# Kernel optimization log

Measured on AMD Instinct MI355X. Metric: run time of the kernel, lower is better.

## Reference

```python
import jax, jax.numpy as jnp
import numpy as np

E, G, NL, NC, NLP, NPTS = 256, 8, 4, 6, 6, 13
GD = E // G
FIX_SCALE = jnp.array([[0,0,0],[0.45,0,0],[-0.45,0,0],[0,0.45,0],[0,-0.45,0],[0,0,0.45],[0,0,-0.45]], dtype=jnp.float32)
FM_SHAPES = [(64,176),(32,88),(16,44),(8,22)]

def linear(x, w, b):
    return x @ w + b

def layernorm(x, g, b):
    m = x.mean(-1, keepdims=True)
    v = ((x - m) ** 2).mean(-1, keepdims=True)
    return (x - m) * jax.lax.rsqrt(v + 1e-5) * g + b

def grid_sample_bilinear(fm, grid):
    # fm: [B,C,H,W], grid: [B,Hg,Wg,2] in [-1,1]; align_corners=False, zero padding
    B, C, H, W = fm.shape
    gx = (grid[..., 0] + 1.0) * (W * 0.5) - 0.5
    gy = (grid[..., 1] + 1.0) * (H * 0.5) - 0.5
    x0f = jnp.floor(gx); y0f = jnp.floor(gy)
    wx1 = gx - x0f; wy1 = gy - y0f
    x0 = x0f.astype(jnp.int32); y0 = y0f.astype(jnp.int32)
    def samp(fmb, x, y):
        valid = ((x >= 0) & (x < W) & (y >= 0) & (y < H)).astype(fmb.dtype)
        xc = jnp.clip(x, 0, W - 1); yc = jnp.clip(y, 0, H - 1)
        return fmb[:, yc, xc] * valid[None]
    def per_batch(fmb, x0b, y0b, wx1b, wy1b):
        wx0 = 1.0 - wx1b; wy0 = 1.0 - wy1b
        v00 = samp(fmb, x0b, y0b)
        v01 = samp(fmb, x0b + 1, y0b)
        v10 = samp(fmb, x0b, y0b + 1)
        v11 = samp(fmb, x0b + 1, y0b + 1)
        return (v00 * (wx0 * wy0)[None] + v01 * (wx1b * wy0)[None]
                + v10 * (wx0 * wy1b)[None] + v11 * (wx1b * wy1b)[None])
    return jax.vmap(per_batch)(fm, x0, y0, wx1, wy1)

def setup_inputs() -> dict:
    key = jax.random.key(0)
    ks = jax.random.split(key, 32)
    bs, na = 2, 900
    inp = {
        'instance_feature': jax.random.normal(ks[0], (bs, na, E), jnp.float32),
        'anchor': jax.random.normal(ks[1], (bs, na, 11), jnp.float32),
        'anchor_embed': jax.random.normal(ks[2], (bs, na, E), jnp.float32),
        'projection_mat': jax.random.normal(ks[3], (bs, NC, 4, 4), jnp.float32),
        'image_wh': jnp.ones((bs, NC, 2), jnp.float32) * jnp.array([704.0, 256.0]),
    }
    for i, (h, w) in enumerate(FM_SHAPES):
        inp[f'fm{i}'] = jax.random.normal(ks[4 + i], (bs, NC, E, h, w), jnp.float32)
    s = 0.02
    inp['lfc_w'] = s * jax.random.normal(ks[10], (E, NLP * 3), jnp.float32)
    inp['lfc_b'] = jnp.zeros((NLP * 3,), jnp.float32)
    inp['ce1_w'] = s * jax.random.normal(ks[11], (12, E), jnp.float32)
    inp['ce1_b'] = jnp.zeros((E,), jnp.float32)
    inp['ln1_g'] = jnp.ones((E,), jnp.float32)
    inp['ln1_b'] = jnp.zeros((E,), jnp.float32)
    inp['ce2_w'] = s * jax.random.normal(ks[12], (E, E), jnp.float32)
    inp['ce2_b'] = jnp.zeros((E,), jnp.float32)
    inp['ln2_g'] = jnp.ones((E,), jnp.float32)
    inp['ln2_b'] = jnp.zeros((E,), jnp.float32)
    inp['wfc_w'] = s * jax.random.normal(ks[13], (E, G * NL * NPTS), jnp.float32)
    inp['wfc_b'] = jnp.zeros((G * NL * NPTS,), jnp.float32)
    inp['op_w'] = s * jax.random.normal(ks[14], (E, E), jnp.float32)
    inp['op_b'] = jnp.zeros((E,), jnp.float32)
    return inp

def reference(instance_feature, anchor, anchor_embed, fm0, fm1, fm2, fm3,
              projection_mat, image_wh,
              lfc_w, lfc_b, ce1_w, ce1_b, ln1_g, ln1_b, ce2_w, ce2_b,
              ln2_g, ln2_b, wfc_w, wfc_b, op_w, op_b):
    bs, na = instance_feature.shape[:2]
    # ---- keypoint generator ----
    size = jnp.exp(anchor[..., None, 3:6])                      # [bs,na,1,3] (W,L,H)
    kp = FIX_SCALE * size                                       # [bs,na,7,3]
    ls = jax.nn.sigmoid(linear(instance_feature, lfc_w, lfc_b)).reshape(bs, na, NLP, 3) - 0.5
    kp = jnp.concatenate([kp, ls * size], axis=-2)              # [bs,na,13,3]
    sy, cy = anchor[..., 6], anchor[..., 7]
    zero, one = jnp.zeros_like(cy), jnp.ones_like(cy)
    rot = jnp.stack([jnp.stack([cy, -sy, zero], -1),
                     jnp.stack([sy, cy, zero], -1),
                     jnp.stack([zero, zero, one], -1)], axis=-2)  # [bs,na,3,3]
    key_points = jnp.einsum('bnij,bnpj->bnpi', rot, kp) + anchor[..., None, 0:3]
    # ---- weights ----
    feat = instance_feature + anchor_embed
    cam_in = projection_mat[:, :, :3].reshape(bs, NC, 12)
    ce = layernorm(jax.nn.relu(linear(cam_in, ce1_w, ce1_b)), ln1_g, ln1_b)
    ce = layernorm(jax.nn.relu(linear(ce, ce2_w, ce2_b)), ln2_g, ln2_b)   # [bs,nc,E]
    fcam = feat[:, :, None] + ce[:, None]                        # [bs,na,nc,E]
    w = linear(fcam, wfc_w, wfc_b).reshape(bs, na, NC * NL * NPTS, G)
    w = jax.nn.softmax(w, axis=-2).reshape(bs, na, NC, NL, NPTS, G)
    # ---- projection + sampling ----
    pts = jnp.concatenate([key_points, jnp.ones_like(key_points[..., :1])], -1)  # [bs,na,np,4]
    pts2d = jnp.einsum('bcij,bnpj->bcnpi', projection_mat, pts)  # [bs,nc,na,np,4]
    z = jnp.maximum(pts2d[..., 2:3], 1e-5)
    uv = pts2d[..., :2] / z
    uv = uv / image_wh[:, :, None, None]
    grid = (uv * 2.0 - 1.0).reshape(bs * NC, na, NPTS, 2)
    feats = []
    for fm in (fm0, fm1, fm2, fm3):
        h, ww = fm.shape[-2:]
        feats.append(grid_sample_bilinear(fm.reshape(bs * NC, E, h, ww), grid))  # [bs*nc,E,na,np]
    feats = jnp.stack(feats, axis=1).reshape(bs, NC, NL, E, na, NPTS)
    feats = feats.transpose(0, 4, 1, 2, 5, 3)                    # [bs,na,nc,nl,np,E]
    # ---- fusion (sum over cams, levels, pts) ----
    featg = feats.reshape(bs, na, NC, NL, NPTS, G, GD)
    fused = jnp.einsum('bnclpg,bnclpgd->bngd', w, featg).reshape(bs, na, E)
    out = linear(fused, op_w, op_b)
    return jnp.concatenate([out, instance_feature], axis=-1)
```

## Files before the change

kernel.cpp:

```cpp
#include <hip/hip_runtime.h>
#include <hip/hip_bf16.h>

typedef __hip_bfloat16 bf16;
typedef unsigned short ushort_t;
typedef unsigned int uint_t;

#define E    256
#define Gn   8
#define NLv  4
#define NCam 6
#define NP   13
#define BSz  2
#define NA   900
#define NW   416
#define NQ   312
#define NCW  2496

#define NT_BLK   2808
#define PREP_BLK 1800
#define CE_BLK   12

__device__ __forceinline__ float cvt(float v) { return v; }
__device__ __forceinline__ float cvt(bf16 v)  { return __bfloat162float(v); }
__device__ __forceinline__ ushort_t f2us(float v) {
  bf16 h = __float2bfloat16(v);
  return *(ushort_t*)&h;
}
__device__ __forceinline__ float blo(uint_t d) { return __uint_as_float(d << 16); }
__device__ __forceinline__ float bhi(uint_t d) { return __uint_as_float(d & 0xffff0000u); }
__device__ __forceinline__ bool is_f32(const void* wh) {
  return *(const uint_t*)wh == 0x44300000u;
}

constexpr float FIXS[7][3] = {
    {0.f,0.f,0.f},{0.45f,0.f,0.f},{-0.45f,0.f,0.f},
    {0.f,0.45f,0.f},{0.f,-0.45f,0.f},{0.f,0.f,0.45f},{0.f,0.f,-0.45f}};
__constant__ int LH_c[4]  = {64,32,16,8};
__constant__ int LW_c[4]  = {176,88,44,22};
__constant__ int LHW_c[4] = {11264,2816,704,176};
__constant__ int PXB_c[4] = {0,135168,168960,177408};
__constant__ size_t TB_c[4]  = {0ull, 34603008ull, 43253760ull, 45416448ull};

struct CEShared {
  float cin[12];
  float xs[E];
  float red[E];
};

template<typename T>
__device__ void camembed_bce_body(CEShared* sm, int bc,
    const T* __restrict__ pm,
    const T* __restrict__ ce1_w, const T* __restrict__ ce1_b,
    const T* __restrict__ ln1_g, const T* __restrict__ ln1_b,
    const T* __restrict__ ce2_w, const T* __restrict__ ce2_b,
    const T* __restrict__ ln2_g, const T* __restrict__ ln2_b,
    const T* __restrict__ wfc_w, float* __restrict__ bce) {
  const int t  = threadIdx.x;
  float* cin = sm->cin; float* xs = sm->xs; float* red = sm->red;
  if (t < 12) cin[t] = cvt(pm[bc*16 + t]);
  __syncthreads();
  float h = cvt(ce1_b[t]);
#pragma unroll
  for (int k = 0; k < 12; ++k) h = fmaf(cin[k], cvt(ce1_w[k*E + t]), h);
  h = fmaxf(h, 0.f);
  red[t] = h; __syncthreads();
  for (int off = 128; off > 0; off >>= 1) { if (t < off) red[t] += red[t+off]; __syncthreads(); }
  float m = red[0] * (1.f/E); __syncthreads();
  float d = h - m;
  red[t] = d*d; __syncthreads();
  for (int off = 128; off > 0; off >>= 1) { if (t < off) red[t] += red[t+off]; __syncthreads(); }
  float v = red[0] * (1.f/E); __syncthreads();
  xs[t] = d * rsqrtf(v + 1e-5f) * cvt(ln1_g[t]) + cvt(ln1_b[t]);
  __syncthreads();
  float h2 = cvt(ce2_b[t]);
  for (int k = 0; k < E; ++k) h2 = fmaf(xs[k], cvt(ce2_w[k*E + t]), h2);
  h2 = fmaxf(h2, 0.f);
  red[t] = h2; __syncthreads();
  for (int off = 128; off > 0; off >>= 1) { if (t < off) red[t] += red[t+off]; __syncthreads(); }
  float m2 = red[0] * (1.f/E); __syncthreads();
  float d2 = h2 - m2;
  red[t] = d2*d2; __syncthreads();
  for (int off = 128; off > 0; off >>= 1) { if (t < off) red[t] += red[t+off]; __syncthreads(); }
  float v2 = red[0] * (1.f/E);
  __syncthreads();
  xs[t] = d2 * rsqrtf(v2 + 1e-5f) * cvt(ln2_g[t]) + cvt(ln2_b[t]);
  __syncthreads();
  for (int j = t; j < NW; j += E) {
    float s = 0.f;
    for (int k = 0; k < E; ++k) s = fmaf(xs[k], cvt(wfc_w[(size_t)k*NW + j]), s);
    bce[bc*NW + j] = s;
  }
}

struct alignas(16) PWShared2 {
  float rec[NQ*8];
  float instL[E];
  float feat[E];
  float P[96];
  float whs[12];
  float anc[11];
  float ls[18];
};

template<typename T>
__device__ void prep_body(PWShared2* sm, int bn,
    const T* __restrict__ inst, const T* __restrict__ anchor,
    const T* __restrict__ aemb, const T* __restrict__ pm, const T* __restrict__ wh,
    const T* __restrict__ lfc_w, const T* __restrict__ lfc_b,
    const T* __restrict__ wfc_w, const T* __restrict__ wfc_b,
    float* __restrict__ recs_g, float* __restrict__ A_g) {
  const int b = bn / NA;
  const int t = threadIdx.x;
  float* instL = sm->instL; float* feat = sm->feat;
  float* rec = sm->rec; float* P = sm->P; float* whs = sm->whs;
  float* anc = sm->anc; float* ls = sm->ls;

  const float iv = cvt(inst[(size_t)bn*E + t]);
  instL[t] = iv;
  feat[t]  = iv + cvt(aemb[(size_t)bn*E + t]);
  if (t < 96)        P[t]       = cvt(pm[(size_t)b*96 + t]);
  else if (t < 108)  whs[t-96]  = cvt(wh[(size_t)b*12 + (t-96)]);
  else if (t < 119)  anc[t-108] = cvt(anchor[(size_t)bn*11 + (t-108)]);
  __syncthreads();

  {
    float a00=0.f, a01=0.f, a02=0.f, a03=0.f;
    float a10=0.f, a11=0.f, a12=0.f, a13=0.f;
    const bool two = (t < NW - E);
    for (int k = 0; k < E; k += 4) {
      const float f0 = feat[k], f1 = feat[k+1], f2 = feat[k+2], f3 = feat[k+3];
      a00 = fmaf(f0, cvt(wfc_w[(size_t)(k+0)*NW + t]), a00);
      a01 = fmaf(f1, cvt(wfc_w[(size_t)(k+1)*NW + t]), a01);
      a02 = fmaf(f2, cvt(wfc_w[(size_t)(k+2)*NW + t]), a02);
      a03 = fmaf(f3, cvt(wfc_w[(size_t)(k+3)*NW + t]), a03);
      if (two) {
        a10 = fmaf(f0, cvt(wfc_w[(size_t)(k+0)*NW + E + t]), a10);
        a11 = fmaf(f1, cvt(wfc_w[(size_t)(k+1)*NW + E + t]), a11);
        a12 = fmaf(f2, cvt(wfc_w[(size_t)(k+2)*NW + E + t]), a12);
        a13 = fmaf(f3, cvt(wfc_w[(size_t)(k+3)*NW + E + t]), a13);
      }
    }
    A_g[(size_t)bn*NW + t] = (a00+a01) + (a02+a03) + cvt(wfc_b[t]);
    if (two) A_g[(size_t)bn*NW + E + t] = (a10+a11) + (a12+a13) + cvt(wfc_b[E + t]);
  }
  if (t < 18) {
    float s = cvt(lfc_b[t]);
#pragma unroll 8
    for (int k = 0; k < E; ++k) s = fmaf(instL[k], cvt(lfc_w[(size_t)k*18 + t]), s);
    ls[t] = 1.f/(1.f + expf(-s)) - 0.5f;
  }
  __syncthreads();

  if (t < NP) {
    const float s0 = expf(anc[3]), s1 = expf(anc[4]), s2 = expf(anc[5]);
    float kx, ky, kz;
    if (t < 7) { kx = FIXS[t][0]*s0; ky = FIXS[t][1]*s1; kz = FIXS[t][2]*s2; }
    else { const int q = (t-7)*3; kx = ls[q]*s0; ky = ls[q+1]*s1; kz = ls[q+2]*s2; }
    const float sy = anc[6], cy = anc[7];
    const float wx = cy*kx - sy*ky + anc[0];
    const float wy = sy*kx + cy*ky + anc[1];
    const float wz = kz + anc[2];
    for (int c = 0; c < NCam; ++c) {
      const float* Pc = &P[c*16];
      const float px = Pc[0]*wx + Pc[1]*wy + Pc[2]*wz  + Pc[3];
      const float py = Pc[4]*wx + Pc[5]*wy + Pc[6]*wz  + Pc[7];
      const float pz = Pc[8]*wx + Pc[9]*wy + Pc[10]*wz + Pc[11];
      const float z  = fmaxf(pz, 1e-5f);
      const float u  = px / z / whs[c*2+0];
      const float v  = py / z / whs[c*2+1];
#pragma unroll
      for (int l = 0; l < NLv; ++l) {
        const int Wl_ = LW_c[l], Hl = LH_c[l];
        const float fx = u * (float)Wl_ - 0.5f;
        const float fy = v * (float)Hl  - 0.5f;
        const float x0f = floorf(fx), y0f = floorf(fy);
        const int x0 = (int)x0f, y0 = (int)y0f;
        const float wx1 = fx - x0f, wy1 = fy - y0f;
        const float wx0 = 1.f - wx1, wy0 = 1.f - wy1;
        const bool vx0 = (x0 >= 0) && (x0 < Wl_);
        const bool vx1 = (x0+1 >= 0) && (x0+1 < Wl_);
        const bool vy0 = (y0 >= 0) && (y0 < Hl);
        const bool vy1 = (y0+1 >= 0) && (y0+1 < Hl);
        const int x0c = min(max(x0,0),Wl_-1), x1c = min(max(x0+1,0),Wl_-1);
        const int y0c = min(max(y0,0),Hl-1),  y1c = min(max(y0+1,0),Hl-1);
        const int bpx = PXB_c[l] + (b*NCam + c)*LHW_c[l];
        float* r = &rec[((c*NLv + l)*NP + t)*8];
        ((int*)r)[0] = bpx + y0c*Wl_ + x0c;
        ((int*)r)[1] = bpx + y0c*Wl_ + x1c;
        ((int*)r)[2] = bpx + y1c*Wl_ + x0c;
        ((int*)r)[3] = bpx + y1c*Wl_ + x1c;
        r[4] = (vx0 && vy0) ? wx0*wy0 : 0.f;
        r[5] = (vx1 && vy0) ? wx1*wy0 : 0.f;
        r[6] = (vx0 && vy1) ? wx0*wy1 : 0.f;
        r[7] = (vx1 && vy1) ? wx1*wy1 : 0.f;
      }
    }
  }
  __syncthreads();

  float* ro = recs_g + (size_t)bn * (NQ*8);
  for (int i = t; i < NQ*2; i += 256)
    ((float4*)ro)[i] = ((const float4*)rec)[i];
}

struct TRShared { ushort_t tile[64][64]; };

template<typename T>
__device__ void transpose_tile(TRShared* sm, const T* __restrict__ fm,
                               bf16* __restrict__ tfm, int HW, int bc, int p0) {
  const int t = threadIdx.x;
  ushort_t (*tile)[64] = sm->tile;
  ushort_t* tfmu = (ushort_t*)tfm;
  const int sub = t & 15;
  const int grp = t >> 4;
  const int pq  = p0 + sub*4;
  const bool pv = (pq < HW);
#pragma unroll
  for (int cb = 0; cb < 4; ++cb) {
#pragma unroll
    for (int j = 0; j < 4; ++j) {
      const int chl = grp + j*16;
      const int ch  = cb*64 + chl;
      ushort4 v;
      if (pv) {
        const size_t base = (size_t)(bc*E + ch)*HW + pq;
        if constexpr (sizeof(T) == 2) {
          v = *(const ushort4*)((const ushort_t*)fm + base);
        } else {
          const float4 vf = *(const float4*)((const float*)fm + base);
          v.x = f2us(vf.x); v.y = f2us(vf.y); v.z = f2us(vf.z); v.w = f2us(vf.w);
        }
      } else {
        v.x = 0; v.y = 0; v.z = 0; v.w = 0;
      }
      const int qw = sub ^ ((chl >> 2) & 7);
      *(ushort4*)&tile[chl][qw << 2] = v;
    }
    __syncthreads();
    const int ch4 = sub << 2;
    const int swz = sub & 7;
#pragma unroll
    for (int j = 0; j < 4; ++j) {
      const int pxl = grp + j*16;
      const int p = p0 + pxl;
      if (p < HW) {
        const int col = (((pxl >> 2) ^ swz) << 2) + (pxl & 3);
        ushort4 o;
        o.x = tile[ch4+0][col];
        o.y = tile[ch4+1][col];
        o.z = tile[ch4+2][col];
        o.w = tile[ch4+3][col];
        *(ushort4*)(tfmu + ((size_t)bc*HW + p)*E + cb*64 + ch4) = o;
      }
    }
    __syncthreads();
  }
}

__device__ __forceinline__ void tr_decode(int g, int& lvl, int& bc, int& tile) {
  if (g < 2112)      { lvl = 0; bc = g / 176; tile = g - bc*176; }
  else if (g < 2640) { g -= 2112; lvl = 1; bc = g / 44; tile = g - bc*44; }
  else if (g < 2772) { g -= 2640; lvl = 2; bc = g / 11; tile = g - bc*11; }
  else               { g -= 2772; lvl = 3; bc = g / 3;  tile = g - bc*3; }
}

struct alignas(16) FusedSM {
  union { TRShared tr; PWShared2 pw; CEShared ce; } u;
};

__global__ __launch_bounds__(256) void k_stage_all(
    const void* inst, const void* anchor, const void* aemb, const void* pm, const void* wh,
    const void* fm0, const void* fm1, const void* fm2, const void* fm3,
    const void* lfc_w, const void* lfc_b,
    const void* ce1_w, const void* ce1_b, const void* ln1_g, const void* ln1_b,
    const void* ce2_w, const void* ce2_b, const void* ln2_g, const void* ln2_b,
    const void* wfc_w, const void* wfc_b,
    bf16* tfm, float* recs_g, float* A_g, float* bce) {
  __shared__ FusedSM sm;
  const bool f32 = is_f32(wh);
  const int g = blockIdx.x;
  if (g < CE_BLK) {
    if (f32)
      camembed_bce_body<float>(&sm.u.ce, g, (const float*)pm, (const float*)ce1_w,
        (const float*)ce1_b, (const float*)ln1_g, (const float*)ln1_b,
        (const float*)ce2_w, (const float*)ce2_b, (const float*)ln2_g,
        (const float*)ln2_b, (const float*)wfc_w, bce);
    else
      camembed_bce_body<bf16>(&sm.u.ce, g, (const bf16*)pm, (const bf16*)ce1_w,
        (const bf16*)ce1_b, (const bf16*)ln1_g, (const bf16*)ln1_b,
        (const bf16*)ce2_w, (const bf16*)ce2_b, (const bf16*)ln2_g,
        (const bf16*)ln2_b, (const bf16*)wfc_w, bce);
    return;
  }
  const int gi = g - CE_BLK;
  bool isT; int idx;
  if (gi < 4500) {
    const int grp = gi / 5, r = gi - grp*5;
    if (r < 3) { isT = true;  idx = grp*3 + r; }
    else       { isT = false; idx = grp*2 + (r - 3); }
  } else {
    isT = true; idx = 2700 + (gi - 4500);
  }
  if (isT) {
    int lvl, bc, tile;
    tr_decode(idx, lvl, bc, tile);
    const void* fms[4] = {fm0, fm1, fm2, fm3};
    const void* fm = fms[lvl];
    const int HW = LHW_c[lvl];
    bf16* out = tfm + TB_c[lvl];
    if (f32) transpose_tile<float>(&sm.u.tr, (const float*)fm, out, HW, bc, tile*64);
    else     transpose_tile<bf16>(&sm.u.tr, (const bf16*)fm, out, HW, bc, tile*64);
  } else {
    if (f32)
      prep_body<float>(&sm.u.pw, idx, (const float*)inst, (const float*)anchor,
        (const float*)aemb, (const float*)pm, (const float*)wh,
        (const float*)lfc_w, (const float*)lfc_b,
        (const float*)wfc_w, (const float*)wfc_b, recs_g, A_g);
    else
      prep_body<bf16>(&sm.u.pw, idx, (const bf16*)inst, (const bf16*)anchor,
        (const bf16*)aemb, (const bf16*)pm, (const bf16*)wh,
        (const bf16*)lfc_w, (const bf16*)lfc_b,
        (const bf16*)wfc_w, (const bf16*)wfc_b, recs_g, A_g);
  }
}

struct alignas(16) GOShared2 {
  float rec[NQ*8];
  float Wl[NCW];
  float red4f[8*E];
  float red[512];
  float inv8[8];
};

template<typename T>
__device__ void gather_body2(GOShared2* sm,
    const float* __restrict__ recs, const float* __restrict__ A_g,
    const float* __restrict__ bce, const bf16* __restrict__ tfm,
    const T* __restrict__ inst, const T* __restrict__ op_w, const T* __restrict__ op_b,
    T* __restrict__ outp) {
  const int bn = blockIdx.x; const int b = bn / NA;
  const int t = threadIdx.x; const int lane = t & 63; const int wv = t >> 6;
  const int g8 = lane >> 3; const int gg = t & 7;
  float* rec = sm->rec; float* Wl = sm->Wl;
  float* red4f = sm->red4f; float* red = sm->red; float* inv8 = sm->inv8;

  {
    const float* rsrc = recs + (size_t)bn * (NQ*8);
    for (int i = t; i < NQ*2; i += 512) ((float4*)rec)[i] = ((const float4*)rsrc)[i];
    const float* Ab = A_g + (size_t)bn * NW;
    const float* bb = bce + (size_t)(b*NCam) * NW;
    for (int f = t; f < NCW; f += 512) {
      const int c = f / NW, j = f - c*NW;
      Wl[f] = Ab[j] + bb[c*NW + j];
    }
  }
  __syncthreads();

  float mx = -1e30f;
  for (int f = t; f < NCW; f += 512) mx = fmaxf(mx, Wl[f]);
  red[t] = mx; __syncthreads();
  for (int off = 256; off >= 8; off >>= 1) { if (t < off) red[t] = fmaxf(red[t], red[t+off]); __syncthreads(); }
  const float mg = red[gg]; __syncthreads();
  float sum = 0.f;
  for (int f = t; f < NCW; f += 512) { const float e = expf(Wl[f] - mg); Wl[f] = e; sum += e; }
  red[t] = sum; __syncthreads();
  for (int off = 256; off >= 8; off >>= 1) { if (t < off) red[t] += red[t+off]; __syncthreads(); }
  if (t < 8) inv8[t] = 1.f / red[t];
  __syncthreads();

  const ushort_t* tf = (const ushort_t*)tfm;
  const uint_t chg = (uint_t)(lane * 4);
  const float invg = inv8[g8];
  float a0 = 0.f, a1 = 0.f, a2 = 0.f, a3 = 0.f;
  int qi = wv;
  int4   off = *(const int4*)(&rec[qi*8]);
  float4 cw  = *(const float4*)(&rec[qi*8 + 4]);
  float  eq  = Wl[qi*8 + g8];
#pragma unroll 2
  for (int i = 0; i < 39; ++i) {
    const uint2 s00 = *(const uint2*)(tf + ((uint_t)off.x*256u + chg));
    const uint2 s01 = *(const uint2*)(tf + ((uint_t)off.y*256u + chg));
    const uint2 s10 = *(const uint2*)(tf + ((uint_t)off.z*256u + chg));
    const uint2 s11 = *(const uint2*)(tf + ((uint_t)off.w*256u + chg));
    const float c0 = cw.x*eq, c1 = cw.y*eq, c2 = cw.z*eq, c3 = cw.w*eq;
    if (i + 1 < 39) {
      const int qn = qi + 8;
      off = *(const int4*)(&rec[qn*8]);
      cw  = *(const float4*)(&rec[qn*8 + 4]);
      eq  = Wl[qn*8 + g8];
      qi = qn;
    }
    a0 = fmaf(c0, blo(s00.x), a0); a0 = fmaf(c1, blo(s01.x), a0);
    a0 = fmaf(c2, blo(s10.x), a0); a0 = fmaf(c3, blo(s11.x), a0);
    a1 = fmaf(c0, bhi(s00.x), a1); a1 = fmaf(c1, bhi(s01.x), a1);
    a1 = fmaf(c2, bhi(s10.x), a1); a1 = fmaf(c3, bhi(s11.x), a1);
    a2 = fmaf(c0, blo(s00.y), a2); a2 = fmaf(c1, blo(s01.y), a2);
    a2 = fmaf(c2, blo(s10.y), a2); a2 = fmaf(c3, blo(s11.y), a2);
    a3 = fmaf(c0, bhi(s00.y), a3); a3 = fmaf(c1, bhi(s01.y), a3);
    a3 = fmaf(c2, bhi(s10.y), a3); a3 = fmaf(c3, bhi(s11.y), a3);
  }
  a0 *= invg; a1 *= invg; a2 *= invg; a3 *= invg;
  *(float4*)&red4f[(wv << 8) + (lane << 2)] = make_float4(a0, a1, a2, a3);
  __syncthreads();

  if (t < E) {
    float fl = red4f[t];
#pragma unroll
    for (int k = 1; k < 8; ++k) fl += red4f[k*E + t];
    red[t] = fl;
  }
  __syncthreads();
  if (t < E) {
    float o0=0.f, o1=0.f, o2=0.f, o3=0.f;
    for (int k = 0; k < E; k += 4) {
      o0 = fmaf(red[k+0], cvt(op_w[(size_t)(k+0)*E + t]), o0);
      o1 = fmaf(red[k+1], cvt(op_w[(size_t)(k+1)*E + t]), o1);
      o2 = fmaf(red[k+2], cvt(op_w[(size_t)(k+2)*E + t]), o2);
      o3 = fmaf(red[k+3], cvt(op_w[(size_t)(k+3)*E + t]), o3);
    }
    const float o = (o0+o1) + (o2+o3) + cvt(op_b[t]);
    outp[(size_t)bn*512 + t] = (T)o;
  } else {
    const int tt = t - E;
    outp[(size_t)bn*512 + E + tt] = inst[(size_t)bn*E + tt];
  }
}

__global__ __launch_bounds__(512, 6) void k_gather_out2(
    const float* recs, const float* A_g, const float* bce, const bf16* tfm,
    const void* inst, const void* op_w, const void* op_b, const void* wh,
    void* outp) {
  __shared__ GOShared2 sm;
  if (is_f32(wh))
    gather_body2<float>(&sm, recs, A_g, bce, tfm, (const float*)inst,
                        (const float*)op_w, (const float*)op_b, (float*)outp);
  else
    gather_body2<bf16>(&sm, recs, A_g, bce, tfm, (const bf16*)inst,
                       (const bf16*)op_w, (const bf16*)op_b, (bf16*)outp);
}

__global__ __launch_bounds__(256) void k_camembed_bce(
    const void* pm, const void* ce1_w, const void* ce1_b,
    const void* ln1_g, const void* ln1_b, const void* ce2_w, const void* ce2_b,
    const void* ln2_g, const void* ln2_b, const void* wfc_w,
    const void* wh, float* bce) {
  __shared__ CEShared sm;
  if (is_f32(wh))
    camembed_bce_body<float>(&sm, blockIdx.x, (const float*)pm,(const float*)ce1_w,(const float*)ce1_b,
      (const float*)ln1_g,(const float*)ln1_b,(const float*)ce2_w,(const float*)ce2_b,
      (const float*)ln2_g,(const float*)ln2_b,(const float*)wfc_w, bce);
  else
    camembed_bce_body<bf16>(&sm, blockIdx.x, (const bf16*)pm,(const bf16*)ce1_w,(const bf16*)ce1_b,
      (const bf16*)ln1_g,(const bf16*)ln1_b,(const bf16*)ce2_w,(const bf16*)ce2_b,
      (const bf16*)ln2_g,(const bf16*)ln2_b,(const bf16*)wfc_w, bce);
}

__global__ __launch_bounds__(256) void k_transpose_all(
    const void* fm0, const void* fm1, const void* fm2, const void* fm3,
    bf16* tfm, const void* wh) {
  __shared__ TRShared sm;
  int lvl, bc, tile;
  tr_decode(blockIdx.x, lvl, bc, tile);
  const void* fms[4] = {fm0, fm1, fm2, fm3};
  const void* fm = fms[lvl];
  const int HW = LHW_c[lvl];
  bf16* out = tfm + TB_c[lvl];
  if (is_f32(wh)) transpose_tile<float>(&sm, (const float*)fm, out, HW, bc, tile*64);
  else            transpose_tile<bf16>(&sm, (const bf16*)fm, out, HW, bc, tile*64);
}

struct alignas(16) MFShared {
  float rec[NQ*8];
  float Wl[NCW];
  float WT[NCW];
  float feat[E];
  float A[NW];
  float red[E];
  float fusedl[E];
  float P[96];
  float whs[12];
  float anc[11];
  float ls[18];
};

__device__ __forceinline__ float gatherT_f(
    const float* __restrict__ rec, const float* __restrict__ wrowbase,
    const bf16* __restrict__ tfm, int b, int t) {
  float acc = 0.f;
  for (int c = 0; c < NCam; ++c) {
#pragma unroll
    for (int l = 0; l < NLv; ++l) {
      const float* wrow = wrowbase + (c*NLv + l)*NP;
      const float* rb   = rec + (c*NLv + l)*NP*8;
      const int HWl = LHW_c[l];
      const bf16* base = tfm + TB_c[l] + ((size_t)(b*NCam + c) * HWl) * E + t;
#pragma unroll
      for (int p = 0; p < NP; ++p) {
        const int4   off = *(const int4*)(rb + p*8);
        const float4 cw  = *(const float4*)(rb + p*8 + 4);
        const float v = cw.x*cvt(base[(size_t)off.x*E]) + cw.y*cvt(base[(size_t)off.y*E])
                      + cw.z*cvt(base[(size_t)off.z*E]) + cw.w*cvt(base[(size_t)off.w*E]);
        acc = fmaf(wrow[p], v, acc);
      }
    }
  }
  return acc;
}

template<typename T>
__device__ __forceinline__ float gatherD_f(
    const float* __restrict__ rec, const float* __restrict__ wrowbase,
    const T* __restrict__ f0, const T* __restrict__ f1,
    const T* __restrict__ f2, const T* __restrict__ f3, int b, int t) {
  const T* fms[4] = {f0, f1, f2, f3};
  float acc = 0.f;
  for (int c = 0; c < NCam; ++c) {
#pragma unroll
    for (int l = 0; l < NLv; ++l) {
      const float* wrow = wrowbase + (c*NLv + l)*NP;
      const float* rb   = rec + (c*NLv + l)*NP*8;
      const int HWl = LHW_c[l];
      const T* base = fms[l] + ((size_t)(b*NCam + c)*E + t) * HWl;
#pragma unroll
      for (int p = 0; p < NP; ++p) {
        const int4   off = *(const int4*)(rb + p*8);
        const float4 cw  = *(const float4*)(rb + p*8 + 4);
        const float v = cw.x*cvt(base[off.x]) + cw.y*cvt(base[off.y])
                      + cw.z*cvt(base[off.z]) + cw.w*cvt(base[off.w]);
        acc = fmaf(wrow[p], v, acc);
      }
    }
  }
  return acc;
}

template<typename T, bool TRANS>
__device__ void main_body(MFShared* sm,
    const T* __restrict__ inst, const T* __restrict__ anchor,
    const T* __restrict__ aemb, const T* __restrict__ pm, const T* __restrict__ wh,
    const T* __restrict__ fm0, const T* __restrict__ fm1,
    const T* __restrict__ fm2, const T* __restrict__ fm3,
    const T* __restrict__ lfc_w, const T* __restrict__ lfc_b,
    const T* __restrict__ wfc_w, const T* __restrict__ wfc_b,
    const T* __restrict__ op_w, const T* __restrict__ op_b,
    const float* __restrict__ bce, const bf16* __restrict__ tfm,
    T* __restrict__ outp) {
  const int bn = blockIdx.x, b = bn / NA, t = threadIdx.x;
  float* anc = sm->anc; float* P = sm->P; float* whs = sm->whs; float* ls = sm->ls;
  float* rec = sm->rec; float* feat = sm->feat; float* A = sm->A;
  float* Wl = sm->Wl; float* WT = sm->WT; float* red = sm->red; float* fusedl = sm->fusedl;

  feat[t] = cvt(inst[(size_t)bn*E + t]) + cvt(aemb[(size_t)bn*E + t]);
  if (t < 96)               P[t]       = cvt(pm[(size_t)b*96 + t]);
  else if (t < 108)         whs[t-96]  = cvt(wh[(size_t)b*12 + (t-96)]);
  else if (t < 119)         anc[t-108] = cvt(anchor[(size_t)bn*11 + (t-108)]);
  if (t >= 128 && t < 146) {
    const int j = t - 128;
    float s = cvt(lfc_b[j]);
    for (int k = 0; k < E; ++k)
      s = fmaf(cvt(inst[(size_t)bn*E + k]), cvt(lfc_w[(size_t)k*18 + j]), s);
    ls[j] = 1.f/(1.f + expf(-s)) - 0.5f;
  }
  __syncthreads();
  {
    float a0 = cvt(wfc_b[t]);
    for (int k = 0; k < E; ++k) a0 = fmaf(feat[k], cvt(wfc_w[(size_t)k*NW + t]), a0);
    A[t] = a0;
    if (t < NW - E) {
      float a1 = cvt(wfc_b[E + t]);
      for (int k = 0; k < E; ++k) a1 = fmaf(feat[k], cvt(wfc_w[(size_t)k*NW + E + t]), a1);
      A[E + t] = a1;
    }
  }
  if (t < NP) {
    const float s0 = expf(anc[3]), s1 = expf(anc[4]), s2 = expf(anc[5]);
    float kx, ky, kz;
    if (t < 7) { kx = FIXS[t][0]*s0; ky = FIXS[t][1]*s1; kz = FIXS[t][2]*s2; }
    else { const int q = (t-7)*3; kx = ls[q]*s0; ky = ls[q+1]*s1; kz = ls[q+2]*s2; }
    const float sy = anc[6], cy = anc[7];
    const float wx = cy*kx - sy*ky + anc[0];
    const float wy = sy*kx + cy*ky + anc[1];
    const float wz = kz + anc[2];
    for (int c = 0; c < NCam; ++c) {
      const float* Pc = &P[c*16];
      const float px = Pc[0]*wx + Pc[1]*wy + Pc[2]*wz  + Pc[3];
      const float py = Pc[4]*wx + Pc[5]*wy + Pc[6]*wz  + Pc[7];
      const float pz = Pc[8]*wx + Pc[9]*wy + Pc[10]*wz + Pc[11];
      const float z  = fmaxf(pz, 1e-5f);
      const float u  = px / z / whs[c*2+0];
      const float v  = py / z / whs[c*2+1];
#pragma unroll
      for (int l = 0; l < NLv; ++l) {
        const int Wl_ = LW_c[l], Hl = LH_c[l];
        const float fx = u * (float)Wl_ - 0.5f;
        const float fy = v * (float)Hl  - 0.5f;
        const float x0f = floorf(fx), y0f = floorf(fy);
        const int x0 = (int)x0f, y0 = (int)y0f;
        const float wx1 = fx - x0f, wy1 = fy - y0f;
        const float wx0 = 1.f - wx1, wy0 = 1.f - wy1;
        const bool vx0 = (x0 >= 0) && (x0 < Wl_);
        const bool vx1 = (x0+1 >= 0) && (x0+1 < Wl_);
        const bool vy0 = (y0 >= 0) && (y0 < Hl);
        const bool vy1 = (y0+1 >= 0) && (y0+1 < Hl);
        const int x0c = min(max(x0,0),Wl_-1), x1c = min(max(x0+1,0),Wl_-1);
        const int y0c = min(max(y0,0),Hl-1),  y1c = min(max(y0+1,0),Hl-1);
        float* r = &rec[((c*NLv + l)*NP + t)*8];
        ((int*)r)[0] = y0c*Wl_ + x0c;
        ((int*)r)[1] = y0c*Wl_ + x1c;
        ((int*)r)[2] = y1c*Wl_ + x0c;
        ((int*)r)[3] = y1c*Wl_ + x1c;
        r[4] = (vx0 && vy0) ? wx0*wy0 : 0.f;
        r[5] = (vx1 && vy0) ? wx1*wy0 : 0.f;
        r[6] = (vx0 && vy1) ? wx0*wy1 : 0.f;
        r[7] = (vx1 && vy1) ? wx1*wy1 : 0.f;
      }
    }
  }
  __syncthreads();
  for (int f = t; f < NCW; f += E) {
    const int c = f / NW, j = f - c*NW;
    Wl[f] = A[j] + bce[(b*NCam + c)*NW + j];
  }
  __syncthreads();
  const int g = t & 7, s = t >> 3;
  float mx = -1e30f;
  for (int q = s; q < NQ; q += 32) mx = fmaxf(mx, Wl[q*8 + g]);
  red[t] = mx; __syncthreads();
  for (int off = 128; off >= 8; off >>= 1) { if (t < off) red[t] = fmaxf(red[t], red[t+off]); __syncthreads(); }
  const float mg = red[g]; __syncthreads();
  float sum = 0.f;
  for (int q = s; q < NQ; q += 32) { const float e = expf(Wl[q*8+g] - mg); Wl[q*8+g] = e; sum += e; }
  red[t] = sum; __syncthreads();
  for (int off = 128; off >= 8; off >>= 1) { if (t < off) red[t] += red[t+off]; __syncthreads(); }
  const float inv = 1.f / red[g]; __syncthreads();
  for (int q = s; q < NQ; q += 32) WT[g*NQ + q] = Wl[q*8+g] * inv;
  __syncthreads();
  const int gg = t >> 5;
  const float* wrowbase = &WT[gg*NQ];
  float acc;
  if (TRANS) acc = gatherT_f(rec, wrowbase, tfm, b, t);
  else       acc = gatherD_f<T>(rec, wrowbase, fm0, fm1, fm2, fm3, b, t);
  fusedl[t] = acc;
  __syncthreads();
  float o = cvt(op_b[t]);
  for (int k = 0; k < E; ++k) o = fmaf(fusedl[k], cvt(op_w[(size_t)k*E + t]), o);
  outp[(size_t)bn*512 + t]     = (T)o;
  outp[(size_t)bn*512 + E + t] = inst[(size_t)bn*E + t];
}

template<bool TRANS>
__global__ __launch_bounds__(256) void k_main_fused(
    const void* inst, const void* anchor, const void* aemb, const void* pm,
    const void* wh, const void* fm0, const void* fm1, const void* fm2,
    const void* fm3, const void* lfc_w, const void* lfc_b, const void* wfc_w,
    const void* wfc_b, const void* op_w, const void* op_b,
    const float* bce, const bf16* tfm, void* outp) {
  __shared__ MFShared sm;
  if (is_f32(wh))
    main_body<float, TRANS>(&sm,(const float*)inst,(const float*)anchor,(const float*)aemb,
      (const float*)pm,(const float*)wh,(const float*)fm0,(const float*)fm1,
      (const float*)fm2,(const float*)fm3,(const float*)lfc_w,(const float*)lfc_b,
      (const float*)wfc_w,(const float*)wfc_b,(const float*)op_w,(const float*)op_b,
      bce, tfm, (float*)outp);
  else
    main_body<bf16, TRANS>(&sm,(const bf16*)inst,(const bf16*)anchor,(const bf16*)aemb,
      (const bf16*)pm,(const bf16*)wh,(const bf16*)fm0,(const bf16*)fm1,
      (const bf16*)fm2,(const bf16*)fm3,(const bf16*)lfc_w,(const bf16*)lfc_b,
      (const bf16*)wfc_w,(const bf16*)wfc_b,(const bf16*)op_w,(const bf16*)op_b,
      bce, tfm, (bf16*)outp);
}

extern "C" void kernel_launch(void* const* d_in, const int* in_sizes, int n_in,
                              void* d_out, int out_size, void* d_ws, size_t ws_size,
                              hipStream_t stream) {
  const void* inst   = d_in[0];
  const void* anchor = d_in[1];
  const void* aemb   = d_in[2];
  const void* pm     = d_in[3];
  const void* wh     = d_in[4];
  const void* fm[4]  = {d_in[5], d_in[6], d_in[7], d_in[8]};
  const void* lfc_w = d_in[9];
  const void* lfc_b = d_in[10];
  const void* ce1_w = d_in[11];
  const void* ce1_b = d_in[12];
  const void* ln1_g = d_in[13];
  const void* ln1_b = d_in[14];
  const void* ce2_w = d_in[15];
  const void* ce2_b = d_in[16];
  const void* ln2_g = d_in[17];
  const void* ln2_b = d_in[18];
  const void* wfc_w = d_in[19];
  const void* wfc_b = d_in[20];
  const void* op_w  = d_in[21];
  const void* op_b  = d_in[22];

  char* wsb = (char*)d_ws;
  float* bce   = (float*)(wsb + 16384);
  float* A_g   = (float*)(wsb + 65536);
  float* recs  = (float*)(wsb + 65536 + 2995200);
  bf16*  tfm_full = (bf16*)(wsb + 65536 + 2995200 + 17971200);
  const size_t need_full = 65536ull + 2995200ull + 17971200ull + 91914240ull;
  bf16*  tfm_small = (bf16*)(wsb + 65536);
  const size_t need_trans = 65536ull + 91914240ull;

  if (ws_size >= need_full) {
    k_stage_all<<<CE_BLK + NT_BLK + PREP_BLK, 256, 0, stream>>>(
        inst, anchor, aemb, pm, wh, fm[0], fm[1], fm[2], fm[3],
        lfc_w, lfc_b, ce1_w, ce1_b, ln1_g, ln1_b, ce2_w, ce2_b, ln2_g, ln2_b,
        wfc_w, wfc_b, tfm_full, recs, A_g, bce);
    k_gather_out2<<<BSz*NA, 512, 0, stream>>>(recs, A_g, bce, tfm_full,
                                              inst, op_w, op_b, wh, d_out);
  } else if (ws_size >= need_trans) {
    k_camembed_bce<<<12, 256, 0, stream>>>(pm, ce1_w, ce1_b, ln1_g, ln1_b,
                                           ce2_w, ce2_b, ln2_g, ln2_b, wfc_w,
                                           wh, bce);
    k_transpose_all<<<2808, 256, 0, stream>>>(fm[0], fm[1], fm[2], fm[3],
                                              tfm_small, wh);
    k_main_fused<true><<<BSz*NA, 256, 0, stream>>>(inst, anchor, aemb, pm, wh,
        fm[0], fm[1], fm[2], fm[3], lfc_w, lfc_b, wfc_w, wfc_b, op_w, op_b,
        bce, tfm_small, d_out);
  } else {
    k_camembed_bce<<<12, 256, 0, stream>>>(pm, ce1_w, ce1_b, ln1_g, ln1_b,
                                           ce2_w, ce2_b, ln2_g, ln2_b, wfc_w,
                                           wh, bce);
    k_main_fused<false><<<BSz*NA, 256, 0, stream>>>(inst, anchor, aemb, pm, wh,
        fm[0], fm[1], fm[2], fm[3], lfc_w, lfc_b, wfc_w, wfc_b, op_w, op_b,
        bce, nullptr, d_out);
  }
}
```

Before: 436.0 us.

## Transpose full 256-channel tile in one pass with 16-byte LDS stores

The feature-map transpose now loads all 256 channels for a 64-pixel tile into registers, writes them into a 64x256 LDS tile with an XOR swizzle, and then emits full 16-byte output stores per thread. This replaces four 64-channel passes that each needed two barriers and 8-byte writes. The goal is fewer synchronisations and wider global writes. In exchange the tile needs 32 KB of LDS (up from 8 KB) and more registers, and launch bounds now request 5 blocks per multiprocessor, which may cause register spills.

```diff
diff --git a/kernel.cpp b/kernel.cpp
--- a/kernel.cpp
+++ b/kernel.cpp
@@ -203,57 +203,56 @@
     ((float4*)ro)[i] = ((const float4*)rec)[i];
 }
 
-struct TRShared { ushort_t tile[64][64]; };
+struct TRShared { ushort_t tileT[64][256]; };
 
 template<typename T>
 __device__ void transpose_tile(TRShared* sm, const T* __restrict__ fm,
                                bf16* __restrict__ tfm, int HW, int bc, int p0) {
   const int t = threadIdx.x;
-  ushort_t (*tile)[64] = sm->tile;
   ushort_t* tfmu = (ushort_t*)tfm;
   const int sub = t & 15;
   const int grp = t >> 4;
   const int pq  = p0 + sub*4;
   const bool pv = (pq < HW);
-#pragma unroll
-  for (int cb = 0; cb < 4; ++cb) {
-#pragma unroll
-    for (int j = 0; j < 4; ++j) {
-      const int chl = grp + j*16;
-      const int ch  = cb*64 + chl;
-      ushort4 v;
-      if (pv) {
-        const size_t base = (size_t)(bc*E + ch)*HW + pq;
-        if constexpr (sizeof(T) == 2) {
-          v = *(const ushort4*)((const ushort_t*)fm + base);
-        } else {
-          const float4 vf = *(const float4*)((const float*)fm + base);
-          v.x = f2us(vf.x); v.y = f2us(vf.y); v.z = f2us(vf.z); v.w = f2us(vf.w);
-        }
+  const int swz = (sub & 7) << 3;
+  const int px0 = sub * 4;
+
+  ushort4 v[16];
+#pragma unroll
+  for (int j = 0; j < 16; ++j) {
+    const int chl = grp + j*16;
+    if (pv) {
+      const size_t base = (size_t)(bc*E + chl)*HW + pq;
+      if constexpr (sizeof(T) == 2) {
+        v[j] = *(const ushort4*)((const ushort_t*)fm + base);
       } else {
-        v.x = 0; v.y = 0; v.z = 0; v.w = 0;
+        const float4 vf = *(const float4*)((const float*)fm + base);
+        v[j].x = f2us(vf.x); v[j].y = f2us(vf.y); v[j].z = f2us(vf.z); v[j].w = f2us(vf.w);
       }
-      const int qw = sub ^ ((chl >> 2) & 7);
-      *(ushort4*)&tile[chl][qw << 2] = v;
-    }
-    __syncthreads();
-    const int ch4 = sub << 2;
-    const int swz = sub & 7;
-#pragma unroll
-    for (int j = 0; j < 4; ++j) {
-      const int pxl = grp + j*16;
-      const int p = p0 + pxl;
-      if (p < HW) {
-        const int col = (((pxl >> 2) ^ swz) << 2) + (pxl & 3);
-        ushort4 o;
-        o.x = tile[ch4+0][col];
-        o.y = tile[ch4+1][col];
-        o.z = tile[ch4+2][col];
-        o.w = tile[ch4+3][col];
-        *(ushort4*)(tfmu + ((size_t)bc*HW + p)*E + cb*64 + ch4) = o;
-      }
-    }
-    __syncthreads();
+    } else {
+      v[j] = make_ushort4(0, 0, 0, 0);
+    }
+  }
+#pragma unroll
+  for (int j = 0; j < 16; ++j) {
+    const int chp = (grp + j*16) ^ swz;
+    sm->tileT[px0+0][chp] = v[j].x;
+    sm->tileT[px0+1][chp] = v[j].y;
+    sm->tileT[px0+2][chp] = v[j].z;
+    sm->tileT[px0+3][chp] = v[j].w;
+  }
+  __syncthreads();
+  const int oct = t & 31;
+  const int pr  = t >> 5;
+#pragma unroll
+  for (int it = 0; it < 8; ++it) {
+    const int pxl = it*8 + pr;
+    const int p = p0 + pxl;
+    if (p < HW) {
+      const int o = oct ^ ((pxl >> 2) & 7);
+      const int4 u = *(const int4*)&sm->tileT[pxl][o << 3];
+      *(int4*)(tfmu + ((size_t)bc*HW + p)*E + (oct << 3)) = u;
+    }
   }
 }
 
@@ -268,7 +267,7 @@
   union { TRShared tr; PWShared2 pw; CEShared ce; } u;
 };
 
-__global__ __launch_bounds__(256) void k_stage_all(
+__global__ __launch_bounds__(256, 5) void k_stage_all(
     const void* inst, const void* anchor, const void* aemb, const void* pm, const void* wh,
     const void* fm0, const void* fm1, const void* fm2, const void* fm3,
     const void* lfc_w, const void* lfc_b,
@@ -455,7 +454,7 @@
       (const bf16*)ln2_g,(const bf16*)ln2_b,(const bf16*)wfc_w, bce);
 }
 
-__global__ __launch_bounds__(256) void k_transpose_all(
+__global__ __launch_bounds__(256, 5) void k_transpose_all(
     const void* fm0, const void* fm1, const void* fm2, const void* fm3,
     bf16* tfm, const void* wh) {
   __shared__ TRShared sm;
```

After: 457.3 us. 1.05x slower.
